# Kernel optimization log

Hardware: AMD Instinct MI355X
Metric: run time of the kernel (lower is better)

The kernel has to match this reference:

```python
import jax, jax.numpy as jnp
import numpy as np

NUM_HEAD = 8
HEAD_SIZE = 32  # attention_size 256 / 8 heads


def setup_inputs() -> dict:
    key = jax.random.key(0)
    ks = jax.random.split(key, 10)
    B, S, H, A = 2, 4096, 256, 256
    x = jax.random.normal(ks[0], (B, S, H), dtype=jnp.float32)
    mask = jax.random.randint(ks[1], (B, S), 0, 2) > 0  # bool key-padding mask
    s = 0.02
    wq = jax.random.normal(ks[2], (A, H), dtype=jnp.float32) * s
    bq = jax.random.normal(ks[3], (A,), dtype=jnp.float32) * s
    wk = jax.random.normal(ks[4], (A, H), dtype=jnp.float32) * s
    bk = jax.random.normal(ks[5], (A,), dtype=jnp.float32) * s
    wv = jax.random.normal(ks[6], (A, H), dtype=jnp.float32) * s
    bv = jax.random.normal(ks[7], (A,), dtype=jnp.float32) * s
    wo = jax.random.normal(ks[8], (H, A), dtype=jnp.float32) * s
    bo = jax.random.normal(ks[9], (H,), dtype=jnp.float32) * s
    return {"x": x, "mask": mask, "wq": wq, "bq": bq, "wk": wk, "bk": bk,
            "wv": wv, "bv": bv, "wo": wo, "bo": bo}


def reference(x, mask, wq, bq, wk, bk, wv, bv, wo, bo):
    B, S, _ = x.shape
    # QKV projections -> [B, S, n_head, head_size]
    q = (x @ wq.T + bq).reshape(B, S, NUM_HEAD, HEAD_SIZE)
    k = (x @ wk.T + bk).reshape(B, S, NUM_HEAD, HEAD_SIZE)
    v = (x @ wv.T + bv).reshape(B, S, NUM_HEAD, HEAD_SIZE)
    # scores [B, H, Sq, Sk]
    attn = jnp.einsum('bqhd,bkhd->bhqk', q, k) / jnp.sqrt(
        jnp.asarray(HEAD_SIZE, dtype=x.dtype))
    # attn*mask - 1e5*~mask  ==  where(mask, attn, -1e5)
    attn = jnp.where(mask[:, None, None, :], attn, jnp.asarray(-100000.0, dtype=x.dtype))
    p = jax.nn.softmax(attn, axis=-1)
    o = jnp.einsum('bhqk,bkhd->bqhd', p, v).reshape(B, S, NUM_HEAD * HEAD_SIZE)
    return o @ wo.T + bo
```

## Files before the change

kernel.cpp:

```cpp
#include <hip/hip_runtime.h>

#define DEV __device__ __forceinline__

typedef __attribute__((ext_vector_type(8)))  short bf16x8;
typedef __attribute__((ext_vector_type(4)))  short s16x4;
typedef __attribute__((ext_vector_type(16))) float f32x16;

constexpr int SB = 2;
constexpr int SS = 4096;
constexpr int SH = 256;
constexpr int NHEAD = 8, HD = 32;
constexpr int M_TOK = SB * SS;
constexpr int NQKV = 3 * SH;

constexpr size_t OFF_CNT  = 0;
constexpr size_t OFF_BIAS = 256;
constexpr size_t OFF_XB   = OFF_BIAS + 32768;
constexpr size_t OFF_WQKV = OFF_XB + (size_t)M_TOK * SH * 2;
constexpr size_t OFF_BQKV = OFF_WQKV + (size_t)NQKV * SH * 2;
constexpr size_t OFF_WOB  = OFF_BQKV + 4096;
constexpr size_t OFF_BO   = OFF_WOB + (size_t)SH * SH * 2;
constexpr size_t OFF_Q    = OFF_BO + 1024;
constexpr size_t OFF_K    = OFF_Q + (size_t)M_TOK * SH * 2;
constexpr size_t OFF_V    = OFF_K + (size_t)M_TOK * SH * 2;
constexpr size_t OFF_VT   = OFF_V + (size_t)M_TOK * SH * 2;
constexpr size_t OFF_O    = OFF_VT + (size_t)M_TOK * SH * 2;
constexpr size_t WS_NEED  = OFF_O + (size_t)M_TOK * SH * 2;

DEV short f2bf(float f) {
  unsigned u = __builtin_bit_cast(unsigned, f);
  u = (u + 0x7FFFu + ((u >> 16) & 1u)) >> 16;
  return (short)u;
}

DEV float bf2f(short s) {
  return __builtin_bit_cast(float, ((unsigned)(unsigned short)s) << 16);
}

DEV float exp2_(float x) {
#if __has_builtin(__builtin_amdgcn_exp2f)
  return __builtin_amdgcn_exp2f(x);
#else
  float r;
  asm("v_exp_f32 %0, %1\n\ts_nop 0" : "=v"(r) : "v"(x));
  return r;
#endif
}

DEV unsigned cvtpk(float lo, float hi) {
  unsigned r;
  asm("v_cvt_pk_bf16_f32 %0, %1, %2" : "=v"(r) : "v"(lo), "v"(hi));
  return r;
}

DEV void plswap(unsigned& a, unsigned& b) {
  asm("v_permlane32_swap_b32 %0, %1" : "+v"(a), "+v"(b));
}

__global__ void prep_kernel(const float* __restrict__ x,
    const float* __restrict__ wq, const float* __restrict__ bq,
    const float* __restrict__ wk, const float* __restrict__ bk,
    const float* __restrict__ wv, const float* __restrict__ bv,
    const float* __restrict__ wo, const float* __restrict__ bo,
    short* __restrict__ xb, short* __restrict__ Wqkv, float* __restrict__ bqkv,
    short* __restrict__ wob, float* __restrict__ bof) {
  const float QS = (float)(1.4426950408889634 / 5.656854249492381);
  long i = (long)blockIdx.x * 256 + threadIdx.x;
  const long NX = (long)M_TOK * SH;
  const long NW = (long)NQKV * SH;
  if (i < NX) { xb[i] = f2bf(x[i]); return; }
  i -= NX;
  if (i < NW) {
    int n = (int)(i >> 8), kk = (int)(i & 255);
    int tn = n >> 8, rr = n & 255;
    const float* src = tn == 0 ? wq : (tn == 1 ? wk : wv);
    float sc = tn == 0 ? QS : 1.f;
    Wqkv[i] = f2bf(src[rr * 256 + kk] * sc);
    return;
  }
  i -= NW;
  if (i < NQKV) {
    int n = (int)i, tn = n >> 8, rr = n & 255;
    const float* src = tn == 0 ? bq : (tn == 1 ? bk : bv);
    float sc = tn == 0 ? QS : 1.f;
    bqkv[n] = src[rr] * sc;
    return;
  }
  i -= NQKV;
  if (i < (long)SH * SH) { wob[i] = f2bf(wo[i]); return; }
  i -= (long)SH * SH;
  if (i < SH) bof[i] = bo[i];
}

template <int MODE>
__global__ __launch_bounds__(256) void gemm_kernel(
    const short* __restrict__ Ag, const short* __restrict__ Bg,
    const float* __restrict__ bias,
    short* __restrict__ q, short* __restrict__ k, short* __restrict__ v,
    float* __restrict__ outf) {
  __shared__ __align__(16) short lA[8192];
  __shared__ __align__(16) short lB[4096];
  const int tid = threadIdx.x;
  const int lane = tid & 63, w = tid >> 6;
  const int wm = w >> 1, wn = w & 1;
  const int hi = lane >> 5, l31 = lane & 31;
  const int mb = blockIdx.x, nb = blockIdx.y;
  f32x16 acc0, acc1;
#pragma unroll
  for (int i = 0; i < 16; ++i) { acc0[i] = 0.f; acc1[i] = 0.f; }
  bf16x8 ra[4], rb[2];
  const int am = tid >> 3, ak = tid & 7;
  auto gload = [&](int kb) {
#pragma unroll
    for (int p = 0; p < 4; ++p)
      ra[p] = *(const bf16x8*)(Ag + (size_t)(mb * 128 + p * 32 + am) * 256 + kb * 64 + ak * 8);
#pragma unroll
    for (int p = 0; p < 2; ++p)
      rb[p] = *(const bf16x8*)(Bg + (size_t)(nb * 64 + p * 32 + am) * 256 + kb * 64 + ak * 8);
  };
  gload(0);
  for (int kb = 0; kb < 4; ++kb) {
    __syncthreads();
#pragma unroll
    for (int p = 0; p < 4; ++p)
      *(bf16x8*)(lA + (ak * 128 + p * 32 + am) * 8) = ra[p];
#pragma unroll
    for (int p = 0; p < 2; ++p)
      *(bf16x8*)(lB + (ak * 64 + p * 32 + am) * 8) = rb[p];
    __syncthreads();
    if (kb < 3) gload(kb + 1);
#pragma unroll
    for (int ks = 0; ks < 4; ++ks) {
      bf16x8 af0 = *(const bf16x8*)(lA + ((2 * ks + hi) * 128 + wm * 64 + l31) * 8);
      bf16x8 af1 = *(const bf16x8*)(lA + ((2 * ks + hi) * 128 + wm * 64 + 32 + l31) * 8);
      bf16x8 bf  = *(const bf16x8*)(lB + ((2 * ks + hi) * 64 + wn * 32 + l31) * 8);
      acc0 = __builtin_amdgcn_mfma_f32_32x32x16_bf16(af0, bf, acc0, 0, 0, 0);
      acc1 = __builtin_amdgcn_mfma_f32_32x32x16_bf16(af1, bf, acc1, 0, 0, 0);
    }
  }
  const int ncol = nb * 64 + wn * 32 + l31;
  const float bval = bias[ncol];
  if (MODE == 0) {
    const int tensor = nb >> 2;
    short* dst = tensor == 0 ? q : (tensor == 1 ? k : v);
    const int a = (nb & 3) * 64 + wn * 32 + l31;
    const int hh = a >> 5, d = a & 31;
#pragma unroll
    for (int mt = 0; mt < 2; ++mt) {
      const f32x16& acc = mt == 0 ? acc0 : acc1;
#pragma unroll
      for (int r = 0; r < 16; ++r) {
        int gm = mb * 128 + wm * 64 + mt * 32 + (r & 3) + 8 * (r >> 2) + 4 * hi;
        int bb = gm >> 12, ss = gm & 4095;
        dst[(((size_t)bb * NHEAD + hh) * SS + ss) * HD + d] = f2bf(acc[r] + bval);
      }
    }
  } else {
#pragma unroll
    for (int mt = 0; mt < 2; ++mt) {
      const f32x16& acc = mt == 0 ? acc0 : acc1;
#pragma unroll
      for (int r = 0; r < 16; ++r) {
        int gm = mb * 128 + wm * 64 + mt * 32 + (r & 3) + 8 * (r >> 2) + 4 * hi;
        outf[(size_t)gm * SH + ncol] = acc[r] + bval;
      }
    }
  }
}

__global__ void scan_mask_kernel(const unsigned char* __restrict__ m,
                                 int* __restrict__ idxC, float* __restrict__ biasC,
                                 int* __restrict__ cnts) {
  __shared__ int f_mis, f_off4, f_3f;
  __shared__ int ts[256];
  const int tid = threadIdx.x, b = blockIdx.x;
  if (tid == 0) { f_mis = 0; f_off4 = 0; f_3f = 0; }
  __syncthreads();
  int lm = 0, lo4 = 0, l3f = 0;
  for (int i = tid; i < 8192; i += 256) {
    unsigned char c = m[i];
    if (c) {
      if (i & 3) lm = 1;
      if ((i & 7) == 4) lo4 = 1;
      if ((i & 3) == 3 && c == 0x3F) l3f = 1;
    }
  }
  if (lm)  atomicOr(&f_mis, 1);
  if (lo4) atomicOr(&f_off4, 1);
  if (l3f) atomicOr(&f_3f, 1);
  __syncthreads();
  const int f = !f_mis ? (f_off4 ? 1 : 3) : (f_3f ? 2 : 0);
  int bits = 0;
  const int rbase = b * 4096 + tid * 16;
#pragma unroll
  for (int j = 0; j < 16; ++j) {
    int r = rbase + j;
    bool on;
    if (f == 0)      on = m[r] != 0;
    else if (f == 1) on = m[(size_t)r * 4] != 0;
    else if (f == 2) on = m[(size_t)r * 4 + 3] != 0;
    else             on = m[(size_t)r * 8] != 0;
    bits |= (int)on << j;
  }
  const int cnt = __popc(bits);
  ts[tid] = cnt;
  __syncthreads();
  for (int off = 1; off < 256; off <<= 1) {
    int u = (tid >= off) ? ts[tid - off] : 0;
    __syncthreads();
    ts[tid] += u;
    __syncthreads();
  }
  const int total = ts[255];
  int pos = ts[tid] - cnt;
  int* idxB = idxC + b * 4096;
  float* biasB = biasC + b * 4096;
  if (total == 0) {
    for (int j = tid; j < 4096; j += 256) { idxB[j] = j; biasB[j] = 0.f; }
    if (tid == 0) cnts[b] = 4096;
    return;
  }
#pragma unroll
  for (int j = 0; j < 16; ++j)
    if ((bits >> j) & 1) { idxB[pos] = tid * 16 + j; biasB[pos] = 0.f; ++pos; }
  int cntpad = (total + 127) & ~127;
  if (cntpad < 128) cntpad = 128;
  for (int j = total + tid; j < cntpad; j += 256) { idxB[j] = -1; biasB[j] = -100000.f; }
  if (tid == 0) cnts[b] = cntpad;
}

__global__ __launch_bounds__(256) void gather_kernel(const short* __restrict__ K,
    const short* __restrict__ V, const int* __restrict__ idxC, const int* __restrict__ cnts,
    short* __restrict__ Kc, short* __restrict__ Vc) {
  const int bh = blockIdx.y, b = bh >> 3;
  const int jb = blockIdx.x * 64;
  if (jb >= cnts[b]) return;
  const int tid = threadIdx.x;
  const int j = jb + (tid >> 2), g = tid & 3;
  const int ix = idxC[b * 4096 + j];
  bf16x8 kv_{}, vv_{};
  if (ix >= 0) {
    kv_ = *(const bf16x8*)(K + ((size_t)bh * SS + ix) * HD + g * 8);
    vv_ = *(const bf16x8*)(V + ((size_t)bh * SS + ix) * HD + g * 8);
  } else {
#pragma unroll
    for (int t = 0; t < 8; ++t) { kv_[t] = 0; vv_[t] = 0; }
  }
  *(bf16x8*)(Kc + ((size_t)bh * SS + j) * HD + g * 8) = kv_;
  *(bf16x8*)(Vc + ((size_t)bh * SS + j) * HD + g * 8) = vv_;
}

__global__ __launch_bounds__(256) void transpose_v_kernel(const short* __restrict__ V,
    const int* __restrict__ cnts, short* __restrict__ Vt) {
  const int bh = blockIdx.x, sbase = blockIdx.y * 64;
  if (sbase >= cnts[bh >> 3]) return;
  __shared__ short t[64][33];
  const int tid = threadIdx.x;
  {
    int s = tid >> 2, g = tid & 3;
    bf16x8 val = *(const bf16x8*)(V + ((size_t)bh * SS + sbase + s) * HD + g * 8);
#pragma unroll
    for (int j = 0; j < 8; ++j) t[s][g * 8 + j] = val[j];
  }
  __syncthreads();
  {
    int d = tid >> 3, gs = tid & 7;
    bf16x8 out;
#pragma unroll
    for (int j = 0; j < 8; ++j) out[j] = t[gs * 8 + j][d];
    *(bf16x8*)(Vt + ((size_t)bh * HD + d) * SS + sbase + gs * 8) = out;
  }
}

__global__ __launch_bounds__(256, 4) void attn_kernel(const short* __restrict__ Q,
    const short* __restrict__ Kc, const short* __restrict__ Vt,
    const float* __restrict__ biasC, const int* __restrict__ cnts,
    short* __restrict__ OP0, short* __restrict__ OP1, float* __restrict__ Lp) {
  __shared__ __align__(16) short sK[4096];
  __shared__ __align__(16) short sV[4096];
  __shared__ __align__(16) float sB[64];
  const int tid = threadIdx.x;
  const int lane = tid & 63, wave = tid >> 6;
  const int hi = lane >> 5, l31 = lane & 31;
  const int qblk = blockIdx.x, bh = blockIdx.y, half = blockIdx.z;
  const int b = bh >> 3, h = bh & 7;
  const int Lh = cnts[b] >> 1;
  const int NIT = Lh >> 6;
  const int kv0 = half * Lh;
  const short* Kb = Kc + ((size_t)bh * SS + kv0) * HD;
  const short* Vb = Vt + (size_t)bh * HD * SS + kv0;
  const float* biasB = biasC + b * SS + kv0;
  const int qbase = qblk * 128 + wave * 32;
  const short* Qrow = Q + ((size_t)bh * SS + qbase + l31) * HD;
  const bf16x8 qf0 = *(const bf16x8*)(Qrow + hi * 8);
  const bf16x8 qf1 = *(const bf16x8*)(Qrow + 16 + hi * 8);
  bf16x8 ones;
#pragma unroll
  for (int j = 0; j < 8; ++j) ones[j] = (short)0x3F80;
  f32x16 accO, lacc;
#pragma unroll
  for (int i = 0; i < 16; ++i) { accO[i] = 0.f; lacc[i] = 0.f; }
  const int kvs = tid >> 2, gd = tid & 3;
  const int dv = tid >> 3, gkv = tid & 7;
  const short* kvsrc = Kb + (size_t)kvs * HD + gd * 8;
  const short* vvsrc = Vb + (size_t)dv * SS + gkv * 8;
  short* kdst = sK + ((size_t)gd * 64 + kvs) * 8;
  short* vdst = sV + ((size_t)gkv * 32 + dv) * 8;
  bf16x8 stgK = *(const bf16x8*)kvsrc;
  bf16x8 stgV = *(const bf16x8*)vvsrc;
  float stgb = (tid < 64) ? biasB[tid] : 0.f;

  for (int kt = 0; kt < NIT; ++kt) {
    __syncthreads();
    *(bf16x8*)kdst = stgK;
    *(bf16x8*)vdst = stgV;
    if (tid < 64) sB[tid] = stgb;
    __syncthreads();
    if (kt + 1 < NIT) {
      stgK = *(const bf16x8*)(kvsrc + (size_t)(kt + 1) * 64 * HD);
      stgV = *(const bf16x8*)(vvsrc + (kt + 1) * 64);
      if (tid < 64) stgb = biasB[(kt + 1) * 64 + tid];
    }
    const float4* bp4 = (const float4*)sB;
    f32x16 s0, s1;
#pragma unroll
    for (int qd = 0; qd < 4; ++qd) {
      float4 f0 = bp4[2 * qd + hi];
      float4 f1 = bp4[8 + 2 * qd + hi];
      s0[4 * qd + 0] = f0.x; s0[4 * qd + 1] = f0.y; s0[4 * qd + 2] = f0.z; s0[4 * qd + 3] = f0.w;
      s1[4 * qd + 0] = f1.x; s1[4 * qd + 1] = f1.y; s1[4 * qd + 2] = f1.z; s1[4 * qd + 3] = f1.w;
    }
    const bf16x8 a00 = *(const bf16x8*)(sK + ((hi)*64 + l31) * 8);
    const bf16x8 a01 = *(const bf16x8*)(sK + ((2 + hi) * 64 + l31) * 8);
    const bf16x8 a10 = *(const bf16x8*)(sK + ((hi)*64 + 32 + l31) * 8);
    const bf16x8 a11 = *(const bf16x8*)(sK + ((2 + hi) * 64 + 32 + l31) * 8);
    s0 = __builtin_amdgcn_mfma_f32_32x32x16_bf16(a00, qf0, s0, 0, 0, 0);
    s0 = __builtin_amdgcn_mfma_f32_32x32x16_bf16(a01, qf1, s0, 0, 0, 0);
    s1 = __builtin_amdgcn_mfma_f32_32x32x16_bf16(a10, qf0, s1, 0, 0, 0);
    s1 = __builtin_amdgcn_mfma_f32_32x32x16_bf16(a11, qf1, s1, 0, 0, 0);
    f32x16 p;
#pragma unroll
    for (int r = 0; r < 16; ++r) p[r] = exp2_(s0[r]);
    bf16x8 pa1, pa2;
    {
      unsigned a0 = cvtpk(p[0], p[1]),   a1 = cvtpk(p[2], p[3]);
      unsigned b0 = cvtpk(p[4], p[5]),   b1 = cvtpk(p[6], p[7]);
      plswap(a0, b0); plswap(a1, b1);
      unsigned c0 = cvtpk(p[8], p[9]),   c1 = cvtpk(p[10], p[11]);
      unsigned d0 = cvtpk(p[12], p[13]), d1 = cvtpk(p[14], p[15]);
      plswap(c0, d0); plswap(c1, d1);
      union { unsigned u[4]; bf16x8 v; } x, y;
      x.u[0] = a0; x.u[1] = a1; x.u[2] = b0; x.u[3] = b1;
      y.u[0] = c0; y.u[1] = c1; y.u[2] = d0; y.u[3] = d1;
      pa1 = x.v; pa2 = y.v;
    }
    const bf16x8 vb0 = *(const bf16x8*)(sV + ((hi)*32 + l31) * 8);
    const bf16x8 vb1 = *(const bf16x8*)(sV + ((2 + hi) * 32 + l31) * 8);
    accO = __builtin_amdgcn_mfma_f32_32x32x16_bf16(pa1, vb0, accO, 0, 0, 0);
    accO = __builtin_amdgcn_mfma_f32_32x32x16_bf16(pa2, vb1, accO, 0, 0, 0);
    lacc = __builtin_amdgcn_mfma_f32_32x32x16_bf16(pa1, ones, lacc, 0, 0, 0);
    lacc = __builtin_amdgcn_mfma_f32_32x32x16_bf16(pa2, ones, lacc, 0, 0, 0);
#pragma unroll
    for (int r = 0; r < 16; ++r) p[r] = exp2_(s1[r]);
    bf16x8 pa3, pa4;
    {
      unsigned a0 = cvtpk(p[0], p[1]),   a1 = cvtpk(p[2], p[3]);
      unsigned b0 = cvtpk(p[4], p[5]),   b1 = cvtpk(p[6], p[7]);
      plswap(a0, b0); plswap(a1, b1);
      unsigned c0 = cvtpk(p[8], p[9]),   c1 = cvtpk(p[10], p[11]);
      unsigned d0 = cvtpk(p[12], p[13]), d1 = cvtpk(p[14], p[15]);
      plswap(c0, d0); plswap(c1, d1);
      union { unsigned u[4]; bf16x8 v; } x, y;
      x.u[0] = a0; x.u[1] = a1; x.u[2] = b0; x.u[3] = b1;
      y.u[0] = c0; y.u[1] = c1; y.u[2] = d0; y.u[3] = d1;
      pa3 = x.v; pa4 = y.v;
    }
    const bf16x8 vb2 = *(const bf16x8*)(sV + ((4 + hi) * 32 + l31) * 8);
    const bf16x8 vb3 = *(const bf16x8*)(sV + ((6 + hi) * 32 + l31) * 8);
    accO = __builtin_amdgcn_mfma_f32_32x32x16_bf16(pa3, vb2, accO, 0, 0, 0);
    accO = __builtin_amdgcn_mfma_f32_32x32x16_bf16(pa4, vb3, accO, 0, 0, 0);
    lacc = __builtin_amdgcn_mfma_f32_32x32x16_bf16(pa3, ones, lacc, 0, 0, 0);
    lacc = __builtin_amdgcn_mfma_f32_32x32x16_bf16(pa4, ones, lacc, 0, 0, 0);
  }
  short* OP = half ? OP1 : OP0;
#pragma unroll
  for (int r = 0; r < 16; ++r) {
    int qq = (r & 3) + 8 * (r >> 2) + 4 * hi;
    int m = b * SS + qbase + qq;
    OP[(size_t)m * SH + h * HD + l31] = f2bf(accO[r]);
    if (l31 == 0) Lp[((size_t)half * 16 + bh) * SS + qbase + qq] = lacc[r];
  }
}

__global__ __launch_bounds__(256) void combine_kernel(const short* __restrict__ P0,
    const short* __restrict__ P1, const float* __restrict__ Lp,
    short* __restrict__ Ow) {
  int t = blockIdx.x * 256 + threadIdx.x;
  int m = t >> 6, c4 = (t & 63) * 4;
  int b = m >> 12, s = m & 4095, h = c4 >> 5;
  s16x4 o0 = *(const s16x4*)(P0 + (size_t)m * SH + c4);
  s16x4 o1 = *(const s16x4*)(P1 + (size_t)m * SH + c4);
  int bh = b * 8 + h;
  float l = Lp[(size_t)bh * SS + s] + Lp[((size_t)16 + bh) * SS + s];
  float rcp = 1.f / l;
  s16x4 out;
#pragma unroll
  for (int j = 0; j < 4; ++j) out[j] = f2bf((bf2f(o0[j]) + bf2f(o1[j])) * rcp);
  *(s16x4*)(Ow + (size_t)m * SH + c4) = out;
}

extern "C" void kernel_launch(void* const* d_in, const int* in_sizes, int n_in,
                              void* d_out, int out_size, void* d_ws, size_t ws_size,
                              hipStream_t stream) {
  (void)in_sizes; (void)n_in; (void)out_size;
  if (ws_size < WS_NEED) return;
  const float* x  = (const float*)d_in[0];
  const unsigned char* mask = (const unsigned char*)d_in[1];
  const float* wq = (const float*)d_in[2];
  const float* bq = (const float*)d_in[3];
  const float* wk = (const float*)d_in[4];
  const float* bk = (const float*)d_in[5];
  const float* wv = (const float*)d_in[6];
  const float* bv = (const float*)d_in[7];
  const float* wo = (const float*)d_in[8];
  const float* bo = (const float*)d_in[9];
  char* ws = (char*)d_ws;
  int*   cnts    = (int*)(ws + OFF_CNT);
  short* xb      = (short*)(ws + OFF_XB);
  short* Wqkv    = (short*)(ws + OFF_WQKV);
  float* bqkv    = (float*)(ws + OFF_BQKV);
  short* wob     = (short*)(ws + OFF_WOB);
  float* bof     = (float*)(ws + OFF_BO);
  short* Qw      = (short*)(ws + OFF_Q);
  short* Kw      = (short*)(ws + OFF_K);
  short* Vw      = (short*)(ws + OFF_V);
  short* Vtw     = (short*)(ws + OFF_VT);
  short* Kc      = (short*)(ws + OFF_XB);
  short* Vc      = (short*)(ws + OFF_O);
  int*   idxC    = (int*)(ws + OFF_WQKV);
  float* biasC   = (float*)(ws + OFF_WQKV + 65536);
  short* OP0     = (short*)(ws + OFF_K);
  short* OP1     = (short*)(ws + OFF_V);
  float* Lp      = (float*)(ws + OFF_O);

  prep_kernel<<<9220, 256, 0, stream>>>(x, wq, bq, wk, bk, wv, bv, wo, bo,
                                        xb, Wqkv, bqkv, wob, bof);
  gemm_kernel<0><<<dim3(64, 12), 256, 0, stream>>>(xb, Wqkv, bqkv, Qw, Kw, Vw, nullptr);
  scan_mask_kernel<<<2, 256, 0, stream>>>(mask, idxC, biasC, cnts);
  gather_kernel<<<dim3(64, 16), 256, 0, stream>>>(Kw, Vw, idxC, cnts, Kc, Vc);
  transpose_v_kernel<<<dim3(16, 64), 256, 0, stream>>>(Vc, cnts, Vtw);
  attn_kernel<<<dim3(32, 16, 2), 256, 0, stream>>>(Qw, Kc, Vtw, biasC, cnts, OP0, OP1, Lp);
  combine_kernel<<<2048, 256, 0, stream>>>(OP0, OP1, Lp, OP0);
  gemm_kernel<1><<<dim3(64, 4), 256, 0, stream>>>(OP0, wob, bof,
                                                  nullptr, nullptr, nullptr, (float*)d_out);
}
```

Measured before the change: 93.31 us.

## Vectorize prep conversion, fuse gather with V transpose, double attention KV tile

The prep kernel now converts eight floats per thread with float4 loads and bf16x8 stores, which cuts the grid size and the per-element indexing overhead. The K/V gather and the V transpose are merged into one kernel, removing a launch and the round trip of the intermediate gathered V buffer. The attention kernel processes 128 keys per iteration instead of 64, which halves the barrier count and deepens the prefetch. To keep whole tiles, the padding granularity rises to 256 keys, so some extra masked keys may be computed.

```diff
diff --git a/kernel.cpp b/kernel.cpp
--- a/kernel.cpp
+++ b/kernel.cpp
@@ -65,31 +65,57 @@
     short* __restrict__ xb, short* __restrict__ Wqkv, float* __restrict__ bqkv,
     short* __restrict__ wob, float* __restrict__ bof) {
   const float QS = (float)(1.4426950408889634 / 5.656854249492381);
-  long i = (long)blockIdx.x * 256 + threadIdx.x;
+  long i = ((long)blockIdx.x * 256 + threadIdx.x) * 8;
   const long NX = (long)M_TOK * SH;
   const long NW = (long)NQKV * SH;
-  if (i < NX) { xb[i] = f2bf(x[i]); return; }
+  if (i < NX) {
+    const float4* s = (const float4*)(x + i);
+    float4 f0 = s[0], f1 = s[1];
+    bf16x8 o;
+    o[0]=f2bf(f0.x); o[1]=f2bf(f0.y); o[2]=f2bf(f0.z); o[3]=f2bf(f0.w);
+    o[4]=f2bf(f1.x); o[5]=f2bf(f1.y); o[6]=f2bf(f1.z); o[7]=f2bf(f1.w);
+    *(bf16x8*)(xb + i) = o;
+    return;
+  }
   i -= NX;
   if (i < NW) {
     int n = (int)(i >> 8), kk = (int)(i & 255);
     int tn = n >> 8, rr = n & 255;
-    const float* src = tn == 0 ? wq : (tn == 1 ? wk : wv);
+    const float* src = (tn == 0 ? wq : (tn == 1 ? wk : wv)) + rr * 256 + kk;
     float sc = tn == 0 ? QS : 1.f;
-    Wqkv[i] = f2bf(src[rr * 256 + kk] * sc);
+    float4 f0 = *(const float4*)src, f1 = *(const float4*)(src + 4);
+    bf16x8 o;
+    o[0]=f2bf(f0.x*sc); o[1]=f2bf(f0.y*sc); o[2]=f2bf(f0.z*sc); o[3]=f2bf(f0.w*sc);
+    o[4]=f2bf(f1.x*sc); o[5]=f2bf(f1.y*sc); o[6]=f2bf(f1.z*sc); o[7]=f2bf(f1.w*sc);
+    *(bf16x8*)(Wqkv + i) = o;
     return;
   }
   i -= NW;
   if (i < NQKV) {
-    int n = (int)i, tn = n >> 8, rr = n & 255;
-    const float* src = tn == 0 ? bq : (tn == 1 ? bk : bv);
-    float sc = tn == 0 ? QS : 1.f;
-    bqkv[n] = src[rr] * sc;
+    int n = (int)i;
+#pragma unroll
+    for (int j = 0; j < 8; ++j) {
+      int nn = n + j, tn = nn >> 8, rr = nn & 255;
+      const float* src = tn == 0 ? bq : (tn == 1 ? bk : bv);
+      bqkv[nn] = src[rr] * (tn == 0 ? QS : 1.f);
+    }
     return;
   }
   i -= NQKV;
-  if (i < (long)SH * SH) { wob[i] = f2bf(wo[i]); return; }
+  if (i < (long)SH * SH) {
+    const float4* s = (const float4*)(wo + i);
+    float4 f0 = s[0], f1 = s[1];
+    bf16x8 o;
+    o[0]=f2bf(f0.x); o[1]=f2bf(f0.y); o[2]=f2bf(f0.z); o[3]=f2bf(f0.w);
+    o[4]=f2bf(f1.x); o[5]=f2bf(f1.y); o[6]=f2bf(f1.z); o[7]=f2bf(f1.w);
+    *(bf16x8*)(wob + i) = o;
+    return;
+  }
   i -= (long)SH * SH;
-  if (i < SH) bof[i] = bo[i];
+  if (i < SH) {
+#pragma unroll
+    for (int j = 0; j < 8; ++j) bof[i + j] = bo[i + j];
+  }
 }
 
 template <int MODE>
@@ -223,53 +249,36 @@
 #pragma unroll
   for (int j = 0; j < 16; ++j)
     if ((bits >> j) & 1) { idxB[pos] = tid * 16 + j; biasB[pos] = 0.f; ++pos; }
-  int cntpad = (total + 127) & ~127;
-  if (cntpad < 128) cntpad = 128;
+  int cntpad = (total + 255) & ~255;
+  if (cntpad < 256) cntpad = 256;
   for (int j = total + tid; j < cntpad; j += 256) { idxB[j] = -1; biasB[j] = -100000.f; }
   if (tid == 0) cnts[b] = cntpad;
 }
 
-__global__ __launch_bounds__(256) void gather_kernel(const short* __restrict__ K,
+__global__ __launch_bounds__(256) void gather_kv_kernel(const short* __restrict__ K,
     const short* __restrict__ V, const int* __restrict__ idxC, const int* __restrict__ cnts,
-    short* __restrict__ Kc, short* __restrict__ Vc) {
+    short* __restrict__ Kc, short* __restrict__ Vt) {
   const int bh = blockIdx.y, b = bh >> 3;
   const int jb = blockIdx.x * 64;
   if (jb >= cnts[b]) return;
-  const int tid = threadIdx.x;
-  const int j = jb + (tid >> 2), g = tid & 3;
-  const int ix = idxC[b * 4096 + j];
-  bf16x8 kv_{}, vv_{};
-  if (ix >= 0) {
-    kv_ = *(const bf16x8*)(K + ((size_t)bh * SS + ix) * HD + g * 8);
-    vv_ = *(const bf16x8*)(V + ((size_t)bh * SS + ix) * HD + g * 8);
-  } else {
-#pragma unroll
-    for (int t = 0; t < 8; ++t) { kv_[t] = 0; vv_[t] = 0; }
-  }
-  *(bf16x8*)(Kc + ((size_t)bh * SS + j) * HD + g * 8) = kv_;
-  *(bf16x8*)(Vc + ((size_t)bh * SS + j) * HD + g * 8) = vv_;
-}
-
-__global__ __launch_bounds__(256) void transpose_v_kernel(const short* __restrict__ V,
-    const int* __restrict__ cnts, short* __restrict__ Vt) {
-  const int bh = blockIdx.x, sbase = blockIdx.y * 64;
-  if (sbase >= cnts[bh >> 3]) return;
   __shared__ short t[64][33];
   const int tid = threadIdx.x;
-  {
-    int s = tid >> 2, g = tid & 3;
-    bf16x8 val = *(const bf16x8*)(V + ((size_t)bh * SS + sbase + s) * HD + g * 8);
-#pragma unroll
-    for (int j = 0; j < 8; ++j) t[s][g * 8 + j] = val[j];
-  }
+  const int s = tid >> 2, g = tid & 3;
+  const int ix = idxC[b * 4096 + jb + s];
+  bf16x8 kvv{}, vvv{};
+  if (ix >= 0) {
+    kvv = *(const bf16x8*)(K + ((size_t)bh * SS + ix) * HD + g * 8);
+    vvv = *(const bf16x8*)(V + ((size_t)bh * SS + ix) * HD + g * 8);
+  }
+  *(bf16x8*)(Kc + ((size_t)bh * SS + jb + s) * HD + g * 8) = kvv;
+#pragma unroll
+  for (int j = 0; j < 8; ++j) t[s][g * 8 + j] = vvv[j];
   __syncthreads();
-  {
-    int d = tid >> 3, gs = tid & 7;
-    bf16x8 out;
-#pragma unroll
-    for (int j = 0; j < 8; ++j) out[j] = t[gs * 8 + j][d];
-    *(bf16x8*)(Vt + ((size_t)bh * HD + d) * SS + sbase + gs * 8) = out;
-  }
+  const int d = tid >> 3, gs = tid & 7;
+  bf16x8 out;
+#pragma unroll
+  for (int j = 0; j < 8; ++j) out[j] = t[gs * 8 + j][d];
+  *(bf16x8*)(Vt + ((size_t)bh * HD + d) * SS + jb + gs * 8) = out;
 }
 
 __global__ __launch_bounds__(256, 4) void attn_kernel(const short* __restrict__ Q,
@@ -278,14 +287,14 @@
     short* __restrict__ OP0, short* __restrict__ OP1, float* __restrict__ Lp) {
   __shared__ __align__(16) short sK[4096];
   __shared__ __align__(16) short sV[4096];
-  __shared__ __align__(16) float sB[64];
+  __shared__ __align__(16) float sB[128];
   const int tid = threadIdx.x;
   const int lane = tid & 63, wave = tid >> 6;
   const int hi = lane >> 5, l31 = lane & 31;
   const int qblk = blockIdx.x, bh = blockIdx.y, half = blockIdx.z;
   const int b = bh >> 3, h = bh & 7;
   const int Lh = cnts[b] >> 1;
-  const int NIT = Lh >> 6;
+  const int NIT = Lh >> 7;
   const int kv0 = half * Lh;
   const short* Kb = Kc + ((size_t)bh * SS + kv0) * HD;
   const short* Vb = Vt + (size_t)bh * HD * SS + kv0;
@@ -304,83 +313,97 @@
   const int dv = tid >> 3, gkv = tid & 7;
   const short* kvsrc = Kb + (size_t)kvs * HD + gd * 8;
   const short* vvsrc = Vb + (size_t)dv * SS + gkv * 8;
-  short* kdst = sK + ((size_t)gd * 64 + kvs) * 8;
-  short* vdst = sV + ((size_t)gkv * 32 + dv) * 8;
-  bf16x8 stgK = *(const bf16x8*)kvsrc;
-  bf16x8 stgV = *(const bf16x8*)vvsrc;
-  float stgb = (tid < 64) ? biasB[tid] : 0.f;
+  short* kdst0 = sK + ((size_t)gd * 128 + kvs) * 8;
+  short* kdst1 = sK + ((size_t)gd * 128 + 64 + kvs) * 8;
+  short* vdst0 = sV + ((size_t)gkv * 32 + dv) * 8;
+  short* vdst1 = sV + ((size_t)(gkv + 8) * 32 + dv) * 8;
+  bf16x8 stgK0 = *(const bf16x8*)kvsrc;
+  bf16x8 stgK1 = *(const bf16x8*)(kvsrc + 64 * HD);
+  bf16x8 stgV0 = *(const bf16x8*)vvsrc;
+  bf16x8 stgV1 = *(const bf16x8*)(vvsrc + 64);
+  float stgb = (tid < 128) ? biasB[tid] : 0.f;
 
   for (int kt = 0; kt < NIT; ++kt) {
     __syncthreads();
-    *(bf16x8*)kdst = stgK;
-    *(bf16x8*)vdst = stgV;
-    if (tid < 64) sB[tid] = stgb;
+    *(bf16x8*)kdst0 = stgK0;
+    *(bf16x8*)kdst1 = stgK1;
+    *(bf16x8*)vdst0 = stgV0;
+    *(bf16x8*)vdst1 = stgV1;
+    if (tid < 128) sB[tid] = stgb;
     __syncthreads();
     if (kt + 1 < NIT) {
-      stgK = *(const bf16x8*)(kvsrc + (size_t)(kt + 1) * 64 * HD);
-      stgV = *(const bf16x8*)(vvsrc + (kt + 1) * 64);
-      if (tid < 64) stgb = biasB[(kt + 1) * 64 + tid];
-    }
-    const float4* bp4 = (const float4*)sB;
-    f32x16 s0, s1;
-#pragma unroll
-    for (int qd = 0; qd < 4; ++qd) {
-      float4 f0 = bp4[2 * qd + hi];
-      float4 f1 = bp4[8 + 2 * qd + hi];
-      s0[4 * qd + 0] = f0.x; s0[4 * qd + 1] = f0.y; s0[4 * qd + 2] = f0.z; s0[4 * qd + 3] = f0.w;
-      s1[4 * qd + 0] = f1.x; s1[4 * qd + 1] = f1.y; s1[4 * qd + 2] = f1.z; s1[4 * qd + 3] = f1.w;
-    }
-    const bf16x8 a00 = *(const bf16x8*)(sK + ((hi)*64 + l31) * 8);
-    const bf16x8 a01 = *(const bf16x8*)(sK + ((2 + hi) * 64 + l31) * 8);
-    const bf16x8 a10 = *(const bf16x8*)(sK + ((hi)*64 + 32 + l31) * 8);
-    const bf16x8 a11 = *(const bf16x8*)(sK + ((2 + hi) * 64 + 32 + l31) * 8);
-    s0 = __builtin_amdgcn_mfma_f32_32x32x16_bf16(a00, qf0, s0, 0, 0, 0);
-    s0 = __builtin_amdgcn_mfma_f32_32x32x16_bf16(a01, qf1, s0, 0, 0, 0);
-    s1 = __builtin_amdgcn_mfma_f32_32x32x16_bf16(a10, qf0, s1, 0, 0, 0);
-    s1 = __builtin_amdgcn_mfma_f32_32x32x16_bf16(a11, qf1, s1, 0, 0, 0);
-    f32x16 p;
-#pragma unroll
-    for (int r = 0; r < 16; ++r) p[r] = exp2_(s0[r]);
-    bf16x8 pa1, pa2;
-    {
-      unsigned a0 = cvtpk(p[0], p[1]),   a1 = cvtpk(p[2], p[3]);
-      unsigned b0 = cvtpk(p[4], p[5]),   b1 = cvtpk(p[6], p[7]);
-      plswap(a0, b0); plswap(a1, b1);
-      unsigned c0 = cvtpk(p[8], p[9]),   c1 = cvtpk(p[10], p[11]);
-      unsigned d0 = cvtpk(p[12], p[13]), d1 = cvtpk(p[14], p[15]);
-      plswap(c0, d0); plswap(c1, d1);
-      union { unsigned u[4]; bf16x8 v; } x, y;
-      x.u[0] = a0; x.u[1] = a1; x.u[2] = b0; x.u[3] = b1;
-      y.u[0] = c0; y.u[1] = c1; y.u[2] = d0; y.u[3] = d1;
-      pa1 = x.v; pa2 = y.v;
-    }
-    const bf16x8 vb0 = *(const bf16x8*)(sV + ((hi)*32 + l31) * 8);
-    const bf16x8 vb1 = *(const bf16x8*)(sV + ((2 + hi) * 32 + l31) * 8);
-    accO = __builtin_amdgcn_mfma_f32_32x32x16_bf16(pa1, vb0, accO, 0, 0, 0);
-    accO = __builtin_amdgcn_mfma_f32_32x32x16_bf16(pa2, vb1, accO, 0, 0, 0);
-    lacc = __builtin_amdgcn_mfma_f32_32x32x16_bf16(pa1, ones, lacc, 0, 0, 0);
-    lacc = __builtin_amdgcn_mfma_f32_32x32x16_bf16(pa2, ones, lacc, 0, 0, 0);
-#pragma unroll
-    for (int r = 0; r < 16; ++r) p[r] = exp2_(s1[r]);
-    bf16x8 pa3, pa4;
-    {
-      unsigned a0 = cvtpk(p[0], p[1]),   a1 = cvtpk(p[2], p[3]);
-      unsigned b0 = cvtpk(p[4], p[5]),   b1 = cvtpk(p[6], p[7]);
-      plswap(a0, b0); plswap(a1, b1);
-      unsigned c0 = cvtpk(p[8], p[9]),   c1 = cvtpk(p[10], p[11]);
-      unsigned d0 = cvtpk(p[12], p[13]), d1 = cvtpk(p[14], p[15]);
-      plswap(c0, d0); plswap(c1, d1);
-      union { unsigned u[4]; bf16x8 v; } x, y;
-      x.u[0] = a0; x.u[1] = a1; x.u[2] = b0; x.u[3] = b1;
-      y.u[0] = c0; y.u[1] = c1; y.u[2] = d0; y.u[3] = d1;
-      pa3 = x.v; pa4 = y.v;
-    }
-    const bf16x8 vb2 = *(const bf16x8*)(sV + ((4 + hi) * 32 + l31) * 8);
-    const bf16x8 vb3 = *(const bf16x8*)(sV + ((6 + hi) * 32 + l31) * 8);
-    accO = __builtin_amdgcn_mfma_f32_32x32x16_bf16(pa3, vb2, accO, 0, 0, 0);
-    accO = __builtin_amdgcn_mfma_f32_32x32x16_bf16(pa4, vb3, accO, 0, 0, 0);
-    lacc = __builtin_amdgcn_mfma_f32_32x32x16_bf16(pa3, ones, lacc, 0, 0, 0);
-    lacc = __builtin_amdgcn_mfma_f32_32x32x16_bf16(pa4, ones, lacc, 0, 0, 0);
+      const short* ks = kvsrc + (size_t)(kt + 1) * 128 * HD;
+      stgK0 = *(const bf16x8*)ks;
+      stgK1 = *(const bf16x8*)(ks + 64 * HD);
+      const short* vs = vvsrc + (kt + 1) * 128;
+      stgV0 = *(const bf16x8*)vs;
+      stgV1 = *(const bf16x8*)(vs + 64);
+      if (tid < 128) stgb = biasB[(kt + 1) * 128 + tid];
+    }
+#pragma unroll
+    for (int sub = 0; sub < 2; ++sub) {
+      const int kb = sub * 64;
+      const float4* bp4 = (const float4*)(sB + kb);
+      f32x16 s0, s1;
+#pragma unroll
+      for (int qd = 0; qd < 4; ++qd) {
+        float4 f0 = bp4[2 * qd + hi];
+        float4 f1 = bp4[8 + 2 * qd + hi];
+        s0[4 * qd + 0] = f0.x; s0[4 * qd + 1] = f0.y; s0[4 * qd + 2] = f0.z; s0[4 * qd + 3] = f0.w;
+        s1[4 * qd + 0] = f1.x; s1[4 * qd + 1] = f1.y; s1[4 * qd + 2] = f1.z; s1[4 * qd + 3] = f1.w;
+      }
+      const bf16x8 a00 = *(const bf16x8*)(sK + ((hi)*128 + kb + l31) * 8);
+      const bf16x8 a01 = *(const bf16x8*)(sK + ((2 + hi) * 128 + kb + l31) * 8);
+      const bf16x8 a10 = *(const bf16x8*)(sK + ((hi)*128 + kb + 32 + l31) * 8);
+      const bf16x8 a11 = *(const bf16x8*)(sK + ((2 + hi) * 128 + kb + 32 + l31) * 8);
+      s0 = __builtin_amdgcn_mfma_f32_32x32x16_bf16(a00, qf0, s0, 0, 0, 0);
+      s0 = __builtin_amdgcn_mfma_f32_32x32x16_bf16(a01, qf1, s0, 0, 0, 0);
+      s1 = __builtin_amdgcn_mfma_f32_32x32x16_bf16(a10, qf0, s1, 0, 0, 0);
+      s1 = __builtin_amdgcn_mfma_f32_32x32x16_bf16(a11, qf1, s1, 0, 0, 0);
+      f32x16 p;
+#pragma unroll
+      for (int r = 0; r < 16; ++r) p[r] = exp2_(s0[r]);
+      bf16x8 pa1, pa2;
+      {
+        unsigned a0 = cvtpk(p[0], p[1]),   a1 = cvtpk(p[2], p[3]);
+        unsigned b0 = cvtpk(p[4], p[5]),   b1 = cvtpk(p[6], p[7]);
+        plswap(a0, b0); plswap(a1, b1);
+        unsigned c0 = cvtpk(p[8], p[9]),   c1 = cvtpk(p[10], p[11]);
+        unsigned d0 = cvtpk(p[12], p[13]), d1 = cvtpk(p[14], p[15]);
+        plswap(c0, d0); plswap(c1, d1);
+        union { unsigned u[4]; bf16x8 v; } x, y;
+        x.u[0] = a0; x.u[1] = a1; x.u[2] = b0; x.u[3] = b1;
+        y.u[0] = c0; y.u[1] = c1; y.u[2] = d0; y.u[3] = d1;
+        pa1 = x.v; pa2 = y.v;
+      }
+      const bf16x8 vb0 = *(const bf16x8*)(sV + ((sub * 8 + hi) * 32 + l31) * 8);
+      const bf16x8 vb1 = *(const bf16x8*)(sV + ((sub * 8 + 2 + hi) * 32 + l31) * 8);
+      accO = __builtin_amdgcn_mfma_f32_32x32x16_bf16(pa1, vb0, accO, 0, 0, 0);
+      accO = __builtin_amdgcn_mfma_f32_32x32x16_bf16(pa2, vb1, accO, 0, 0, 0);
+      lacc = __builtin_amdgcn_mfma_f32_32x32x16_bf16(pa1, ones, lacc, 0, 0, 0);
+      lacc = __builtin_amdgcn_mfma_f32_32x32x16_bf16(pa2, ones, lacc, 0, 0, 0);
+#pragma unroll
+      for (int r = 0; r < 16; ++r) p[r] = exp2_(s1[r]);
+      bf16x8 pa3, pa4;
+      {
+        unsigned a0 = cvtpk(p[0], p[1]),   a1 = cvtpk(p[2], p[3]);
+        unsigned b0 = cvtpk(p[4], p[5]),   b1 = cvtpk(p[6], p[7]);
+        plswap(a0, b0); plswap(a1, b1);
+        unsigned c0 = cvtpk(p[8], p[9]),   c1 = cvtpk(p[10], p[11]);
+        unsigned d0 = cvtpk(p[12], p[13]), d1 = cvtpk(p[14], p[15]);
+        plswap(c0, d0); plswap(c1, d1);
+        union { unsigned u[4]; bf16x8 v; } x, y;
+        x.u[0] = a0; x.u[1] = a1; x.u[2] = b0; x.u[3] = b1;
+        y.u[0] = c0; y.u[1] = c1; y.u[2] = d0; y.u[3] = d1;
+        pa3 = x.v; pa4 = y.v;
+      }
+      const bf16x8 vb2 = *(const bf16x8*)(sV + ((sub * 8 + 4 + hi) * 32 + l31) * 8);
+      const bf16x8 vb3 = *(const bf16x8*)(sV + ((sub * 8 + 6 + hi) * 32 + l31) * 8);
+      accO = __builtin_amdgcn_mfma_f32_32x32x16_bf16(pa3, vb2, accO, 0, 0, 0);
+      accO = __builtin_amdgcn_mfma_f32_32x32x16_bf16(pa4, vb3, accO, 0, 0, 0);
+      lacc = __builtin_amdgcn_mfma_f32_32x32x16_bf16(pa3, ones, lacc, 0, 0, 0);
+      lacc = __builtin_amdgcn_mfma_f32_32x32x16_bf16(pa4, ones, lacc, 0, 0, 0);
+    }
   }
   short* OP = half ? OP1 : OP0;
 #pragma unroll
@@ -436,19 +459,17 @@
   short* Vw      = (short*)(ws + OFF_V);
   short* Vtw     = (short*)(ws + OFF_VT);
   short* Kc      = (short*)(ws + OFF_XB);
-  short* Vc      = (short*)(ws + OFF_O);
   int*   idxC    = (int*)(ws + OFF_WQKV);
   float* biasC   = (float*)(ws + OFF_WQKV + 65536);
   short* OP0     = (short*)(ws + OFF_K);
   short* OP1     = (short*)(ws + OFF_V);
   float* Lp      = (float*)(ws + OFF_O);
 
-  prep_kernel<<<9220, 256, 0, stream>>>(x, wq, bq, wk, bk, wv, bv, wo, bo,
+  prep_kernel<<<1153, 256, 0, stream>>>(x, wq, bq, wk, bk, wv, bv, wo, bo,
                                         xb, Wqkv, bqkv, wob, bof);
   gemm_kernel<0><<<dim3(64, 12), 256, 0, stream>>>(xb, Wqkv, bqkv, Qw, Kw, Vw, nullptr);
   scan_mask_kernel<<<2, 256, 0, stream>>>(mask, idxC, biasC, cnts);
-  gather_kernel<<<dim3(64, 16), 256, 0, stream>>>(Kw, Vw, idxC, cnts, Kc, Vc);
-  transpose_v_kernel<<<dim3(16, 64), 256, 0, stream>>>(Vc, cnts, Vtw);
+  gather_kv_kernel<<<dim3(64, 16), 256, 0, stream>>>(Kw, Vw, idxC, cnts, Kc, Vtw);
   attn_kernel<<<dim3(32, 16, 2), 256, 0, stream>>>(Qw, Kc, Vtw, biasC, cnts, OP0, OP1, Lp);
   combine_kernel<<<2048, 256, 0, stream>>>(OP0, OP1, Lp, OP0);
   gemm_kernel<1><<<dim3(64, 4), 256, 0, stream>>>(OP0, wob, bof,
```

Measured after the change: 90.46 us. 1.03x faster.
